# Kernel optimization log

Hardware: AMD Instinct MI355X
Metric: run time of the kernel (lower is better)

## Reference

```python
import jax, jax.numpy as jnp
import numpy as np
from jax import lax

D_MODEL = 512
D_STATE = 16
D_CONV = 4
EXPAND = 2
D_INNER = EXPAND * D_MODEL
DT_RANK = (D_MODEL + 15) // 16  # ceil(d_model/16) = 32
B = 2
L = 2048


def _silu(x):
    return x * jax.nn.sigmoid(x)


def _mamba_block(x, norm_w, norm_b, in_w, conv_w, conv_b, xproj_w, dt_w, dt_b, A_log, D_skip, out_w):
    # x: [B, L, D_MODEL]; pre-norm residual Mamba block.
    Bsz = x.shape[0]
    mu = x.mean(-1, keepdims=True)
    xc0 = x - mu
    xn = xc0 * lax.rsqrt((xc0 * xc0).mean(-1, keepdims=True) + 1e-5)
    xn = xn * norm_w + norm_b
    # in_proj (no bias): [B, L, 2*D_INNER]
    xz = jnp.einsum('bld,ed->ble', xn, in_w)
    xc, z = jnp.split(xz, 2, axis=-1)
    # depthwise causal conv over time
    xt = xc.transpose(0, 2, 1)  # [B, D_INNER, L]
    xt = lax.conv_general_dilated(xt, conv_w[:, None, :], (1,), [(D_CONV - 1, 0)],
                                  feature_group_count=D_INNER,
                                  dimension_numbers=('NCH', 'OIH', 'NCH'))
    xc = _silu((xt + conv_b[None, :, None]).transpose(0, 2, 1))  # [B, L, D_INNER]
    # x_proj -> (dt, B, C)
    dbc = jnp.einsum('bld,ed->ble', xc, xproj_w)
    dt, Bs, Cs = jnp.split(dbc, [DT_RANK, DT_RANK + D_STATE], axis=-1)
    delta = jax.nn.softplus(jnp.einsum('blr,dr->bld', dt, dt_w) + dt_b)  # [B, L, D_INNER]
    A = -jnp.exp(A_log)  # [D_INNER, D_STATE]

    def step(h, inp):
        d_t, B_t, C_t, u_t = inp  # [B,d], [B,n], [B,n], [B,d]
        h = jnp.exp(d_t[..., None] * A) * h + (d_t * u_t)[..., None] * B_t[:, None, :]
        y_t = jnp.einsum('bdn,bn->bd', h, C_t)
        return h, y_t

    xs = (delta.transpose(1, 0, 2), Bs.transpose(1, 0, 2), Cs.transpose(1, 0, 2), xc.transpose(1, 0, 2))
    h0 = jnp.zeros((Bsz, D_INNER, D_STATE), x.dtype)
    _, ys = lax.scan(step, h0, xs)
    y = ys.transpose(1, 0, 2) + xc * D_skip  # skip connection D*u
    y = y * _silu(z)
    return x + jnp.einsum('ble,de->bld', y, out_w)


def setup_inputs() -> dict:
    key = jax.random.key(0)
    ks = jax.random.split(key, 12)
    f = lambda k, shape, s=0.02: jax.random.normal(k, shape, jnp.float32) * s
    return {
        'v': jax.random.normal(ks[0], (B, L, D_MODEL), jnp.float32),
        'a': jax.random.normal(ks[1], (B, L, D_MODEL), jnp.float32),
        't': jax.random.normal(ks[2], (B, L, D_MODEL), jnp.float32),
        'norm_w': jnp.ones((3, D_MODEL), jnp.float32),
        'norm_b': jnp.zeros((3, D_MODEL), jnp.float32),
        'in_w': f(ks[3], (3, 2 * D_INNER, D_MODEL)),
        'conv_w': f(ks[4], (3, D_INNER, D_CONV), 0.1),
        'conv_b': jnp.zeros((3, D_INNER), jnp.float32),
        'xproj_w': f(ks[5], (3, DT_RANK + 2 * D_STATE, D_INNER)),
        'dt_w': f(ks[6], (3, D_INNER, DT_RANK), 0.1),
        'dt_b': jnp.full((3, D_INNER), -4.6, jnp.float32),  # softplus(-4.6) ~ 0.01
        'A_log': jnp.tile(jnp.log(jnp.arange(1, D_STATE + 1, dtype=jnp.float32)), (3, D_INNER, 1)),
        'D_skip': jnp.ones((3, D_INNER), jnp.float32),
        'out_w': f(ks[7], (3, D_MODEL, D_INNER)),
        'couple_w': f(ks[8], (3, D_MODEL, D_MODEL)),
        'coef': jnp.full((3,), 0.1, jnp.float32),  # alpha, beta, gamma
    }


def reference(v, a, t, norm_w, norm_b, in_w, conv_w, conv_b, xproj_w, dt_w, dt_b, A_log, D_skip, out_w, couple_w, coef):
    # cross-modal residual injection
    v_in = v + coef[0] * jnp.einsum('bld,ed->ble', a, couple_w[0])
    a_in = a + coef[1] * jnp.einsum('bld,ed->ble', t, couple_w[1])
    t_in = t + coef[2] * jnp.einsum('bld,ed->ble', v, couple_w[2])
    x = jnp.stack([v_in, a_in, t_in])  # [3, B, L, D]
    outs = jax.vmap(_mamba_block)(x, norm_w, norm_b, in_w, conv_w, conv_b, xproj_w,
                                  dt_w, dt_b, A_log, D_skip, out_w)
    return (outs[0], outs[1], outs[2])
```

## Files before the change

kernel.cpp:

```cpp
#include <hip/hip_runtime.h>
#include <hip/hip_bf16.h>

#define MODS 3
#define BSZ 2
#define LSEQ 2048
#define DMODEL 512
#define DINNER 1024
#define DTRANK 32
#define NSTATE 16
#define DCONV 4
#define MROWS (BSZ*LSEQ)
#define NCHUNK 64
#define CHUNK 32

#define LOG2E 1.44269504088896f
#define LN2   0.69314718055995f

typedef __attribute__((ext_vector_type(8))) short short8v;
typedef __attribute__((ext_vector_type(4))) short short4v;
typedef __attribute__((ext_vector_type(2))) short short2v;
typedef __attribute__((ext_vector_type(4))) float f32x4;

#if __has_builtin(__builtin_amdgcn_exp2f)
#define EXP2F __builtin_amdgcn_exp2f
#else
#define EXP2F exp2f
#endif
#if __has_builtin(__builtin_amdgcn_rcpf)
#define RCPF __builtin_amdgcn_rcpf
#else
#define RCPF(x) (1.0f / (x))
#endif

__device__ __forceinline__ short f2bf(float x) {
    __hip_bfloat16 h = __float2bfloat16(x);
    return __builtin_bit_cast(short, h);
}
__device__ __forceinline__ float bf2f(short s) {
    return __uint_as_float(((unsigned)(unsigned short)s) << 16);
}
__device__ __forceinline__ void gl_lds16(const short* g, short* l) {
    __builtin_amdgcn_global_load_lds(
        (const __attribute__((address_space(1))) unsigned int*)g,
        (__attribute__((address_space(3))) unsigned int*)l, 16, 0, 0);
}
__device__ __forceinline__ float sigmoid_f(float x) {
    return RCPF(1.f + EXP2F(-x * LOG2E));
}

#define MFMAQ(QR, QC)                                                              \
    _Pragma("unroll")                                                              \
    for (int rf = 0; rf < 2; ++rf)                                                 \
        _Pragma("unroll")                                                          \
        for (int cf = 0; cf < 2; ++cf)                                             \
            _Pragma("unroll")                                                      \
            for (int kh = 0; kh < 2; ++kh)                                         \
                acc[QR][QC][rf][cf] = __builtin_amdgcn_mfma_f32_16x16x32_bf16(     \
                    afr[rf][kh], bfr[cf][kh], acc[QR][QC][rf][cf], 0, 0, 0);

__global__ __launch_bounds__(1024) void gemm8p_inproj(
    const __hip_bfloat16* __restrict__ A_, const __hip_bfloat16* __restrict__ B_,
    __hip_bfloat16* __restrict__ C_)
{
    constexpr int NT = 8;
    __shared__ alignas(16) short As[2 * 16384];
    __shared__ alignas(16) short Bs[2 * 16384];
    const int z = blockIdx.z;
    const int bm0 = blockIdx.x * 256;
    const int bn0 = blockIdx.y * 256;
    const short* Ag = (const short*)A_ + (long)z * 2097152 + (long)bm0 * 512;
    const short* Bg = (const short*)B_ + (long)z * 1048576 + (long)bn0 * 512;
    short* Cg = (short*)C_ + (long)z * 8388608;
    const int tid = threadIdx.x;
    const int lane = tid & 63;
    const int w = tid >> 6;
    const int wr = w >> 2;
    const int wc = w & 3;
    const int lr = lane & 15;
    const int sidx = lane >> 4;
    const int srow_l = tid >> 3;
    const int sgoff = ((tid & 7) ^ (srow_l & 7)) * 8;

    f32x4 acc[2][2][2][2];
    #pragma unroll
    for (int a = 0; a < 2; ++a)
        #pragma unroll
        for (int b = 0; b < 2; ++b)
            #pragma unroll
            for (int c = 0; c < 2; ++c)
                #pragma unroll
                for (int d = 0; d < 2; ++d)
                    acc[a][b][c][d] = (f32x4){0.f, 0.f, 0.f, 0.f};

    short8v afr[2][2];
    short8v bfr[2][2];

    auto stageA = [&](int buf, int half, int t) {
        const int row = half * 128 + srow_l;
        gl_lds16(Ag + (long)row * 512 + t * 64 + sgoff,
                 As + buf * 16384 + half * 8192 + tid * 8);
    };
    auto stageB = [&](int buf, int half, int t) {
        const int row = half * 128 + srow_l;
        gl_lds16(Bg + (long)row * 512 + t * 64 + sgoff,
                 Bs + buf * 16384 + half * 8192 + tid * 8);
    };
    auto loadA = [&](int buf, int qr) {
        #pragma unroll
        for (int rf = 0; rf < 2; ++rf)
            #pragma unroll
            for (int kh = 0; kh < 2; ++kh) {
                const int ra = qr * 128 + wr * 32 + rf * 16 + lr;
                const int g = kh * 4 + sidx;
                afr[rf][kh] = *(const short8v*)&As[buf * 16384 + ra * 64 + ((g ^ (ra & 7)) << 3)];
            }
    };
    auto loadB = [&](int buf, int qc) {
        #pragma unroll
        for (int cf = 0; cf < 2; ++cf)
            #pragma unroll
            for (int kh = 0; kh < 2; ++kh) {
                const int rb = qc * 128 + wc * 32 + cf * 16 + lr;
                const int g = kh * 4 + sidx;
                bfr[cf][kh] = *(const short8v*)&Bs[buf * 16384 + rb * 64 + ((g ^ (rb & 7)) << 3)];
            }
    };

    stageA(0, 0, 0); stageB(0, 0, 0); stageA(0, 1, 0); stageB(0, 1, 0);

    for (int t = 0; t < NT; ++t) {
        const int p = t & 1;
        const bool stg = (t + 1) < NT;
        if (stg) { stageA(p ^ 1, 0, t + 1);
                   asm volatile("s_waitcnt vmcnt(3)" ::: "memory"); }
        else       asm volatile("s_waitcnt vmcnt(2)" ::: "memory");
        asm volatile("s_barrier" ::: "memory");
        loadA(p, 0); loadB(p, 0);
        MFMAQ(0, 0)
        asm volatile("s_barrier" ::: "memory");
        if (stg) { stageB(p ^ 1, 0, t + 1);
                   asm volatile("s_waitcnt vmcnt(3)" ::: "memory"); }
        else       asm volatile("s_waitcnt vmcnt(1)" ::: "memory");
        asm volatile("s_barrier" ::: "memory");
        loadA(p, 1);
        MFMAQ(1, 0)
        asm volatile("s_barrier" ::: "memory");
        if (stg) { stageA(p ^ 1, 1, t + 1);
                   asm volatile("s_waitcnt vmcnt(3)" ::: "memory"); }
        else       asm volatile("s_waitcnt vmcnt(0)" ::: "memory");
        asm volatile("s_barrier" ::: "memory");
        loadB(p, 1);
        MFMAQ(1, 1)
        asm volatile("s_barrier" ::: "memory");
        if (stg) stageB(p ^ 1, 1, t + 1);
        asm volatile("s_barrier" ::: "memory");
        loadA(p, 0);
        MFMAQ(0, 1)
        asm volatile("s_barrier" ::: "memory");
    }

    #pragma unroll
    for (int qr = 0; qr < 2; ++qr)
        #pragma unroll
        for (int qc = 0; qc < 2; ++qc)
            #pragma unroll
            for (int rf = 0; rf < 2; ++rf)
                #pragma unroll
                for (int r = 0; r < 4; ++r) {
                    const int row = bm0 + qr * 128 + wr * 32 + rf * 16 + (lane >> 4) * 4 + r;
                    #pragma unroll
                    for (int cf = 0; cf < 2; ++cf) {
                        const int col = bn0 + qc * 128 + wc * 32 + cf * 16 + lr;
                        Cg[(long)row * 2048 + col] = f2bf(acc[qr][qc][rf][cf][r]);
                    }
                }
}

template<int NJ, int BK>
__global__ __launch_bounds__(256) void gemm_bf16(
    const __hip_bfloat16* __restrict__ A_, const __hip_bfloat16* __restrict__ B_,
    int K, int lda, int ldb, long sA, long sB,
    float* __restrict__ Cf, __hip_bfloat16* __restrict__ Cb, int ldc, long sC,
    const float* __restrict__ res, long sRes,
    const float* __restrict__ resB, const float* __restrict__ resC,
    const __hip_bfloat16* __restrict__ resbf, long sResb,
    const float* __restrict__ coef_base, int coef_stride,
    const float* __restrict__ bias, long sBias, int act)
{
    constexpr int BN = NJ * 32;
    constexpr int ASZ = 128 * BK;
    constexpr int BSZe = BN * BK;
    __shared__ alignas(16) short As[2 * ASZ];
    __shared__ alignas(16) short Bs[2 * BSZe];
    const int z = blockIdx.z;
    const int bm0 = blockIdx.x * 128;
    const int bn0 = blockIdx.y * BN;
    const short* Ag = (const short*)A_ + z * sA + (long)bm0 * lda;
    const short* Bg = (const short*)B_ + z * sB + (long)bn0 * ldb;
    const int tid = threadIdx.x;
    const int lane = tid & 63;
    const int w = tid >> 6;
    const int wr = w >> 1, wc = w & 1;
    const int lr = lane & 15;
    const int sidx = lane >> 4;

    constexpr int SLOTS = BK / 8;
    const int srow = tid / SLOTS;
    const int sslot = tid % SLOTS;
    int swz;
    if constexpr (BK == 64) swz = srow & 7;
    else                    swz = (srow >> 1) & 3;
    const int sgcol = (sslot ^ swz) * 8;
    int fA;
    if constexpr (BK == 64) fA = lr & 7;
    else                    fA = (lr >> 1) & 3;

    constexpr int AINSTR = ASZ / 2048;
    constexpr int BINSTR = BSZe / 2048;
    constexpr int RPI = 2048 / BK;

    f32x4 acc[4][NJ];
    #pragma unroll
    for (int i = 0; i < 4; ++i)
        #pragma unroll
        for (int j = 0; j < NJ; ++j)
            acc[i][j] = (f32x4){0.f, 0.f, 0.f, 0.f};

    auto stage = [&](int buf, int k0) {
        #pragma unroll
        for (int i = 0; i < AINSTR; ++i)
            gl_lds16(Ag + (long)(i * RPI + srow) * lda + k0 + sgcol,
                     As + buf * ASZ + i * 2048 + tid * 8);
        #pragma unroll
        for (int i = 0; i < BINSTR; ++i)
            gl_lds16(Bg + (long)(i * RPI + srow) * ldb + k0 + sgcol,
                     Bs + buf * BSZe + i * 2048 + tid * 8);
    };
    auto compute = [&](int buf) {
        #pragma unroll
        for (int kh = 0; kh < BK / 32; ++kh) {
            const int sl = ((kh * 4 + sidx) ^ fA) * 8;
            short8v af[4], bfr2[NJ];
            #pragma unroll
            for (int i = 0; i < 4; ++i)
                af[i] = *(const short8v*)&As[buf * ASZ + (wr * 64 + i * 16 + lr) * BK + sl];
            #pragma unroll
            for (int j = 0; j < NJ; ++j)
                bfr2[j] = *(const short8v*)&Bs[buf * BSZe + (wc * NJ * 16 + j * 16 + lr) * BK + sl];
            #pragma unroll
            for (int i = 0; i < 4; ++i)
                #pragma unroll
                for (int j = 0; j < NJ; ++j)
                    acc[i][j] = __builtin_amdgcn_mfma_f32_16x16x32_bf16(af[i], bfr2[j], acc[i][j], 0, 0, 0);
        }
    };

    stage(0, 0);
    __syncthreads();
    int cur = 0;
    for (int k0 = BK; k0 < K; k0 += BK) {
        stage(cur ^ 1, k0);
        compute(cur);
        __syncthreads();
        cur ^= 1;
    }
    compute(cur);

    const float alpha = coef_base ? coef_base[z * coef_stride] : 1.0f;
    const float* resz = nullptr;
    if (res) {
        if (resB) resz = (z == 0) ? res : ((z == 1) ? resB : resC);
        else      resz = res + z * sRes;
    }
    const short* resbz = resbf ? (const short*)resbf + (long)z * sResb : nullptr;
    const float* biasz = bias ? bias + z * sBias : nullptr;
    float* Cfz = Cf ? Cf + (long)z * sC : nullptr;
    __hip_bfloat16* Cbz = Cb ? Cb + (long)z * sC : nullptr;
    #pragma unroll
    for (int i = 0; i < 4; ++i) {
        #pragma unroll
        for (int r = 0; r < 4; ++r) {
            const int row = bm0 + wr * 64 + i * 16 + (lane >> 4) * 4 + r;
            #pragma unroll
            for (int j = 0; j < NJ; ++j) {
                const int col = bn0 + wc * NJ * 16 + j * 16 + lr;
                float val = acc[i][j][r];
                if (biasz) val += biasz[col];
                if (act == 1)
                    val = (val > 20.f) ? val : LN2 * __log2f(1.f + EXP2F(val * LOG2E));
                val *= alpha;
                if (resz)  val += resz[(long)row * ldc + col];
                if (resbz) val += bf2f(resbz[(long)row * ldc + col]);
                if (Cfz) Cfz[(long)row * ldc + col] = val;
                else     Cbz[(long)row * ldc + col] = __float2bfloat16(val);
            }
        }
    }
}

__global__ __launch_bounds__(256) void prep_kernel(
    const float* __restrict__ a, const float* __restrict__ t, const float* __restrict__ v,
    __hip_bfloat16* __restrict__ sec_bf,
    const float* __restrict__ couple_w, __hip_bfloat16* __restrict__ cw_bf,
    const float* __restrict__ in_w, __hip_bfloat16* __restrict__ inw_bf,
    const float* __restrict__ xproj_w, __hip_bfloat16* __restrict__ xpw_bf,
    const float* __restrict__ dt_w, __hip_bfloat16* __restrict__ dtw_bf,
    const float* __restrict__ out_w, __hip_bfloat16* __restrict__ outw_bf,
    const float* __restrict__ conv_w, float* __restrict__ cwT,
    const float* __restrict__ A_log, float* __restrict__ A2T)
{
    long idx = (long)blockIdx.x * 256 + threadIdx.x;
    if (idx < 1572864) {
        const int m = (int)(idx >> 19);
        const long off = idx & 524287;
        const float* sec = (m == 0) ? a : (m == 1) ? t : v;
        float4 sv = ((const float4*)sec)[off];
        short4v s;
        s.x = f2bf(sv.x); s.y = f2bf(sv.y); s.z = f2bf(sv.z); s.w = f2bf(sv.w);
        ((short4v*)sec_bf)[idx] = s;
        return;
    }
    idx -= 1572864;
    if (idx < 1449984) {
        const float* s; __hip_bfloat16* d; long off = idx;
        if      (off < 196608)              { s = couple_w; d = cw_bf; }
        else if ((off -= 196608) < 786432)  { s = in_w;     d = inw_bf; }
        else if ((off -= 786432) < 49152)   { s = xproj_w;  d = xpw_bf; }
        else if ((off -= 49152) < 24576)    { s = dt_w;     d = dtw_bf; }
        else    { off -= 24576;               s = out_w;    d = outw_bf; }
        float4 vv = ((const float4*)s)[off];
        short4v o;
        o.x = f2bf(vv.x); o.y = f2bf(vv.y); o.z = f2bf(vv.z); o.w = f2bf(vv.w);
        ((short4v*)d)[off] = o;
        return;
    }
    idx -= 1449984;
    if (idx < 12288) {
        const int k = (int)(idx & 3);
        const int c = (int)((idx >> 2) & 1023);
        const int m = (int)(idx >> 12);
        cwT[(m * DCONV + k) * DINNER + c] = conv_w[idx];
        return;
    }
    idx -= 12288;
    if (idx < 49152) {
        const int c = (int)(idx & 1023);
        const int n = (int)((idx >> 10) & 15);
        const int m = (int)(idx >> 14);
        A2T[idx] = -EXP2F(A_log[((long)m * DINNER + c) * NSTATE + n] * LOG2E) * LOG2E;
    }
}

__global__ __launch_bounds__(256) void ln_kernel(const __hip_bfloat16* __restrict__ x,
                                                 __hip_bfloat16* __restrict__ xn,
                                                 const float* __restrict__ nw, const float* __restrict__ nb)
{
    const int row = blockIdx.x;
    const int m = row >> 12;
    const int tid = threadIdx.x;
    const short2v vv = *(const short2v*)((const short*)x + (long)row * DMODEL + tid * 2);
    const float vx = bf2f(vv.x), vy = bf2f(vv.y);
    float s = vx + vy;
    float sq = vx * vx + vy * vy;
    #pragma unroll
    for (int off = 32; off > 0; off >>= 1) {
        s  += __shfl_down(s, off);
        sq += __shfl_down(sq, off);
    }
    __shared__ float ws_s[4], ws_q[4];
    const int wid = tid >> 6, lane = tid & 63;
    if (lane == 0) { ws_s[wid] = s; ws_q[wid] = sq; }
    __syncthreads();
    if (tid == 0) {
        float ts = ws_s[0] + ws_s[1] + ws_s[2] + ws_s[3];
        float tq = ws_q[0] + ws_q[1] + ws_q[2] + ws_q[3];
        float mu = ts / DMODEL;
        float var = tq / DMODEL - mu * mu;
        ws_s[0] = mu;
        ws_q[0] = rsqrtf(var + 1e-5f);
    }
    __syncthreads();
    const float mu = ws_s[0], rstd = ws_q[0];
    const int e0 = tid * 2;
    float2 w  = *reinterpret_cast<const float2*>(nw + m * DMODEL + e0);
    float2 bb = *reinterpret_cast<const float2*>(nb + m * DMODEL + e0);
    short2v o;
    o.x = f2bf((vx - mu) * rstd * w.x + bb.x);
    o.y = f2bf((vy - mu) * rstd * w.y + bb.y);
    *reinterpret_cast<short2v*>((short*)xn + (long)row * DMODEL + e0) = o;
}

__global__ __launch_bounds__(256) void conv_silu_kernel(const __hip_bfloat16* __restrict__ xz,
    const float* __restrict__ cwT, const float* __restrict__ cb, __hip_bfloat16* __restrict__ xc)
{
    const int idx = blockIdx.x * 256 + threadIdx.x;
    const int c8 = idx & 127;
    const int lt = (idx >> 7) & 255;
    const int mb = idx >> 15;
    const int m  = mb >> 1;
    const int c0 = c8 * 8;
    const int l0 = lt * 8;

    float4 wlo[DCONV], whi[DCONV];
    #pragma unroll
    for (int k = 0; k < DCONV; ++k) {
        wlo[k] = *(const float4*)&cwT[(m * DCONV + k) * DINNER + c0];
        whi[k] = *(const float4*)&cwT[(m * DCONV + k) * DINNER + c0 + 4];
    }
    const float4 blo = *(const float4*)&cb[m * DINNER + c0];
    const float4 bhi = *(const float4*)&cb[m * DINNER + c0 + 4];

    const short* base = (const short*)xz + (long)mb * LSEQ * 2048 + c0;
    short* obase = (short*)xc + (long)mb * LSEQ * DINNER + c0;

    short8v r0 = {}, r1 = {}, r2 = {};
    if (l0 - 3 >= 0) r0 = *(const short8v*)(base + (long)(l0 - 3) * 2048);
    if (l0 - 2 >= 0) r1 = *(const short8v*)(base + (long)(l0 - 2) * 2048);
    if (l0 - 1 >= 0) r2 = *(const short8v*)(base + (long)(l0 - 1) * 2048);

    #pragma unroll
    for (int i = 0; i < 8; ++i) {
        const short8v cur = *(const short8v*)(base + (long)(l0 + i) * 2048);
        float acc[8];
        #pragma unroll
        for (int j = 0; j < 4; ++j) {
            acc[j]     = ((const float*)&blo)[j];
            acc[4 + j] = ((const float*)&bhi)[j];
        }
        #pragma unroll
        for (int j = 0; j < 8; ++j) {
            const float w0 = (j < 4) ? ((const float*)&wlo[0])[j] : ((const float*)&whi[0])[j - 4];
            const float w1 = (j < 4) ? ((const float*)&wlo[1])[j] : ((const float*)&whi[1])[j - 4];
            const float w2 = (j < 4) ? ((const float*)&wlo[2])[j] : ((const float*)&whi[2])[j - 4];
            const float w3 = (j < 4) ? ((const float*)&wlo[3])[j] : ((const float*)&whi[3])[j - 4];
            acc[j] += w0 * bf2f(r0[j]) + w1 * bf2f(r1[j]) + w2 * bf2f(r2[j]) + w3 * bf2f(cur[j]);
        }
        short8v o;
        #pragma unroll
        for (int j = 0; j < 8; ++j)
            o[j] = f2bf(acc[j] * sigmoid_f(acc[j]));
        *(short8v*)(obase + (long)(l0 + i) * DINNER) = o;
        r0 = r1; r1 = r2; r2 = cur;
    }
}

__device__ __forceinline__ bool geo_check(const float* A2) {
    bool g = true;
    #pragma unroll
    for (int n = 1; n < NSTATE; ++n)
        g = g && (__builtin_fabsf(A2[n] - (float)(n + 1) * A2[0]) <= 1e-4f * __builtin_fabsf(A2[n]));
    return g;
}

__global__ __launch_bounds__(256) void scan_pass1_kernel(
    const __hip_bfloat16* __restrict__ delta, const __hip_bfloat16* __restrict__ xc,
    const __hip_bfloat16* __restrict__ dbc, const float* __restrict__ A2T,
    float* __restrict__ Fbuf, float* __restrict__ sumd)
{
    const int bx = blockIdx.x;
    const int chunk = bx & (NCHUNK - 1);
    const int cg = (bx >> 6) & 1;
    const int mb = bx >> 7;
    const int m = mb >> 1, b = mb & 1;
    const int tid = threadIdx.x;
    const int c0 = cg * 256 + tid;
    const int c1 = c0 + 512;

    float A2a[NSTATE], A2b[NSTATE];
    #pragma unroll
    for (int n = 0; n < NSTATE; ++n) {
        A2a[n] = A2T[((long)m * NSTATE + n) * DINNER + c0];
        A2b[n] = A2T[((long)m * NSTATE + n) * DINNER + c1];
    }
    const bool geo = geo_check(A2a) && geo_check(A2b);
    float h0[NSTATE] = {}, h1[NSTATE] = {};
    float sd0 = 0.f, sd1 = 0.f;

    __shared__ float sB[CHUNK][NSTATE];
    const short* dbc_mb = (const short*)dbc + (long)m * MROWS * 64 + (long)b * LSEQ * 64;
    const int t0 = chunk * CHUNK;
    for (int i = tid; i < CHUNK * NSTATE; i += 256) {
        int tt = i >> 4, j = i & 15;
        sB[tt][j] = bf2f(dbc_mb[(long)(t0 + tt) * 64 + 32 + j]);
    }
    __syncthreads();

    const short* dp = (const short*)delta;
    const short* up = (const short*)xc;
    const long base = ((long)mb * LSEQ + t0) * DINNER + c0;
    if (geo) {
        #pragma unroll 2
        for (int tt = 0; tt < CHUNK; ++tt) {
            const long ix = base + (long)tt * DINNER;
            const float d0 = bf2f(dp[ix]),       u0 = bf2f(up[ix]);
            const float d1 = bf2f(dp[ix + 512]), u1 = bf2f(up[ix + 512]);
            const float du0 = d0 * u0, du1 = d1 * u1;
            sd0 += d0; sd1 += d1;
            const float E0 = EXP2F(d0 * A2a[0]);
            const float E1 = EXP2F(d1 * A2b[0]);
            float e0 = 1.f, e1 = 1.f;
            #pragma unroll
            for (int n = 0; n < NSTATE; ++n) {
                e0 *= E0; e1 *= E1;
                h0[n] = e0 * h0[n] + du0 * sB[tt][n];
                h1[n] = e1 * h1[n] + du1 * sB[tt][n];
            }
        }
    } else {
        #pragma unroll 2
        for (int tt = 0; tt < CHUNK; ++tt) {
            const long ix = base + (long)tt * DINNER;
            const float d0 = bf2f(dp[ix]),       u0 = bf2f(up[ix]);
            const float d1 = bf2f(dp[ix + 512]), u1 = bf2f(up[ix + 512]);
            const float du0 = d0 * u0, du1 = d1 * u1;
            sd0 += d0; sd1 += d1;
            #pragma unroll
            for (int n = 0; n < NSTATE; ++n) {
                h0[n] = EXP2F(d0 * A2a[n]) * h0[n] + du0 * sB[tt][n];
                h1[n] = EXP2F(d1 * A2b[n]) * h1[n] + du1 * sB[tt][n];
            }
        }
    }
    const long ob = ((long)mb * NCHUNK + chunk) * (NSTATE * DINNER) + c0;
    #pragma unroll
    for (int n = 0; n < NSTATE; ++n) {
        Fbuf[ob + n * DINNER] = h0[n];
        Fbuf[ob + n * DINNER + 512] = h1[n];
    }
    const long so = (((long)mb * NCHUNK + chunk) << 10) + c0;
    sumd[so] = sd0;
    sumd[so + 512] = sd1;
}

__global__ __launch_bounds__(256) void scan_pass2_kernel(float* __restrict__ Fbuf,
                                                         const float* __restrict__ sumd,
                                                         const float* __restrict__ A2T)
{
    const long idx = (long)blockIdx.x * 256 + threadIdx.x;
    const int mb = (int)(idx >> 14);
    const int cn = (int)(idx & 16383);
    const int n = cn >> 10;
    const int c = cn & 1023;
    const int m = mb >> 1;
    const float A2n = A2T[((long)m * NSTATE + n) * DINNER + c];
    float run = 0.f;
    #pragma unroll 4
    for (int k = 0; k < NCHUNK; ++k) {
        const long o = ((long)(mb * NCHUNK + k) << 14) + cn;
        const float f = Fbuf[o];
        const float p = EXP2F(sumd[(((long)mb * NCHUNK + k) << 10) + c] * A2n);
        Fbuf[o] = run;
        run = p * run + f;
    }
}

__global__ __launch_bounds__(256) void scan_pass3_kernel(
    const __hip_bfloat16* __restrict__ delta, const __hip_bfloat16* __restrict__ xc,
    const __hip_bfloat16* __restrict__ dbc, __hip_bfloat16* __restrict__ xz,
    const float* __restrict__ A2T, const float* __restrict__ D_skip,
    const float* __restrict__ Hin)
{
    const int bx = blockIdx.x;
    const int chunk = bx & (NCHUNK - 1);
    const int cg = (bx >> 6) & 1;
    const int mb = bx >> 7;
    const int m = mb >> 1, b = mb & 1;
    const int tid = threadIdx.x;
    const int c0 = cg * 256 + tid;
    const int c1 = c0 + 512;

    float A2a[NSTATE], A2b[NSTATE];
    #pragma unroll
    for (int n = 0; n < NSTATE; ++n) {
        A2a[n] = A2T[((long)m * NSTATE + n) * DINNER + c0];
        A2b[n] = A2T[((long)m * NSTATE + n) * DINNER + c1];
    }
    const bool geo = geo_check(A2a) && geo_check(A2b);
    const float Dsk0 = D_skip[m * DINNER + c0];
    const float Dsk1 = D_skip[m * DINNER + c1];

    float h0[NSTATE], h1[NSTATE];
    const long ho = ((long)mb * NCHUNK + chunk) * (NSTATE * DINNER) + c0;
    #pragma unroll
    for (int n = 0; n < NSTATE; ++n) {
        h0[n] = Hin[ho + n * DINNER];
        h1[n] = Hin[ho + n * DINNER + 512];
    }

    __shared__ float sBC[CHUNK][2 * NSTATE];
    const short* dbc_mb = (const short*)dbc + (long)m * MROWS * 64 + (long)b * LSEQ * 64;
    const int t0 = chunk * CHUNK;
    for (int i = tid; i < CHUNK * 2 * NSTATE; i += 256) {
        int tt = i >> 5, j = i & 31;
        sBC[tt][j] = bf2f(dbc_mb[(long)(t0 + tt) * 64 + 32 + j]);
    }
    __syncthreads();

    const short* dp = (const short*)delta;
    const short* up = (const short*)xc;
    short* xzp = (short*)xz;
    const long base = ((long)mb * LSEQ + t0) * DINNER + c0;
    const long xbase = ((long)mb * LSEQ + t0) * 2048 + c0;
    if (geo) {
        #pragma unroll 2
        for (int tt = 0; tt < CHUNK; ++tt) {
            const long ix = base + (long)tt * DINNER;
            const long xi = xbase + (long)tt * 2048;
            const float d0 = bf2f(dp[ix]),       u0 = bf2f(up[ix]);
            const float d1 = bf2f(dp[ix + 512]), u1 = bf2f(up[ix + 512]);
            const float zv0 = bf2f(xzp[xi + 1024]);
            const float zv1 = bf2f(xzp[xi + 1536]);
            const float du0 = d0 * u0, du1 = d1 * u1;
            const float E0 = EXP2F(d0 * A2a[0]);
            const float E1 = EXP2F(d1 * A2b[0]);
            float e0 = 1.f, e1 = 1.f;
            float y0 = 0.f, y1 = 0.f;
            #pragma unroll
            for (int n = 0; n < NSTATE; ++n) {
                e0 *= E0; e1 *= E1;
                h0[n] = e0 * h0[n] + du0 * sBC[tt][n];
                h1[n] = e1 * h1[n] + du1 * sBC[tt][n];
                y0 += h0[n] * sBC[tt][16 + n];
                y1 += h1[n] * sBC[tt][16 + n];
            }
            y0 += u0 * Dsk0;
            y1 += u1 * Dsk1;
            xzp[xi]       = f2bf(y0 * (zv0 * sigmoid_f(zv0)));
            xzp[xi + 512] = f2bf(y1 * (zv1 * sigmoid_f(zv1)));
        }
    } else {
        #pragma unroll 2
        for (int tt = 0; tt < CHUNK; ++tt) {
            const long ix = base + (long)tt * DINNER;
            const long xi = xbase + (long)tt * 2048;
            const float d0 = bf2f(dp[ix]),       u0 = bf2f(up[ix]);
            const float d1 = bf2f(dp[ix + 512]), u1 = bf2f(up[ix + 512]);
            const float zv0 = bf2f(xzp[xi + 1024]);
            const float zv1 = bf2f(xzp[xi + 1536]);
            const float du0 = d0 * u0, du1 = d1 * u1;
            float y0 = 0.f, y1 = 0.f;
            #pragma unroll
            for (int n = 0; n < NSTATE; ++n) {
                h0[n] = EXP2F(d0 * A2a[n]) * h0[n] + du0 * sBC[tt][n];
                h1[n] = EXP2F(d1 * A2b[n]) * h1[n] + du1 * sBC[tt][n];
                y0 += h0[n] * sBC[tt][16 + n];
                y1 += h1[n] * sBC[tt][16 + n];
            }
            y0 += u0 * Dsk0;
            y1 += u1 * Dsk1;
            xzp[xi]       = f2bf(y0 * (zv0 * sigmoid_f(zv0)));
            xzp[xi + 512] = f2bf(y1 * (zv1 * sigmoid_f(zv1)));
        }
    }
}

extern "C" void kernel_launch(void* const* d_in, const int* in_sizes, int n_in,
                              void* d_out, int out_size, void* d_ws, size_t ws_size,
                              hipStream_t stream)
{
    const float* v       = (const float*)d_in[0];
    const float* a       = (const float*)d_in[1];
    const float* t       = (const float*)d_in[2];
    const float* norm_w  = (const float*)d_in[3];
    const float* norm_b  = (const float*)d_in[4];
    const float* in_w    = (const float*)d_in[5];
    const float* conv_w  = (const float*)d_in[6];
    const float* conv_b  = (const float*)d_in[7];
    const float* xproj_w = (const float*)d_in[8];
    const float* dt_w    = (const float*)d_in[9];
    const float* dt_b    = (const float*)d_in[10];
    const float* A_log   = (const float*)d_in[11];
    const float* D_skip  = (const float*)d_in[12];
    const float* out_w   = (const float*)d_in[13];
    const float* couple_w= (const float*)d_in[14];
    const float* coef    = (const float*)d_in[15];
    float* out = (float*)d_out;

    typedef __hip_bfloat16 bf;
    float* ws0    = (float*)d_ws;
    bf* x_in_bf   = (bf*)ws0;
    bf* xn_bf     = (bf*)(ws0 + 6291456);
    bf* sec_bf    = xn_bf + 6291456;
    bf* xz_bf     = sec_bf + 6291456;
    bf* xc_bf     = xz_bf + 25165824;
    bf* delta_bf  = xc_bf + 12582912;
    bf* dbc_bf    = delta_bf + 12582912;
    bf* cw_bf     = dbc_bf + 786432;
    bf* inw_bf    = cw_bf + 786432;
    bf* xpw_bf    = inw_bf + 3145728;
    bf* dtw_bf    = xpw_bf + 196608;
    bf* outw_bf   = dtw_bf + 98304;
    float* cwT    = (float*)(outw_bf + 1572864);
    float* A2T    = cwT + 12288;
    float* Fbuf   = A2T + 49152;
    float* sumd   = Fbuf + 6291456;

    dim3 blk(256);

    prep_kernel<<<(1572864 + 1449984 + 12288 + 49152 + 255) / 256, blk, 0, stream>>>(
        a, t, v, sec_bf, couple_w, cw_bf, in_w, inw_bf, xproj_w, xpw_bf,
        dt_w, dtw_bf, out_w, outw_bf, conv_w, cwT, A_log, A2T);

    gemm_bf16<2, 64><<<dim3(32, 8, 3), blk, 0, stream>>>(
        sec_bf, cw_bf, 512, 512, 512, 2097152L, 262144L,
        nullptr, x_in_bf, 512, 2097152L,
        v, 0L, a, t, nullptr, 0L, coef, 1, nullptr, 0L, 0);
    ln_kernel<<<3*4096, blk, 0, stream>>>(x_in_bf, xn_bf, norm_w, norm_b);
    gemm8p_inproj<<<dim3(16, 8, 3), 1024, 0, stream>>>(xn_bf, inw_bf, xz_bf);
    conv_silu_kernel<<<768, blk, 0, stream>>>(xz_bf, cwT, conv_b, xc_bf);
    gemm_bf16<2, 64><<<dim3(32, 1, 3), blk, 0, stream>>>(
        xc_bf, xpw_bf, 1024, 1024, 1024, 4194304L, 65536L,
        nullptr, dbc_bf, 64, 262144L, nullptr, 0L, nullptr, nullptr, nullptr, 0L,
        nullptr, 0, nullptr, 0L, 0);
    gemm_bf16<4, 32><<<dim3(32, 8, 3), blk, 0, stream>>>(
        dbc_bf, dtw_bf, 32, 64, 32, 262144L, 32768L,
        nullptr, delta_bf, 1024, 4194304L, nullptr, 0L, nullptr, nullptr, nullptr, 0L,
        nullptr, 0, dt_b, 1024L, 1);
    scan_pass1_kernel<<<6*2*NCHUNK, blk, 0, stream>>>(delta_bf, xc_bf, dbc_bf, A2T, Fbuf, sumd);
    scan_pass2_kernel<<<(6*1024*16)/256, blk, 0, stream>>>(Fbuf, sumd, A2T);
    scan_pass3_kernel<<<6*2*NCHUNK, blk, 0, stream>>>(delta_bf, xc_bf, dbc_bf, xz_bf,
                                                      A2T, D_skip, Fbuf);
    gemm_bf16<2, 64><<<dim3(32, 8, 3), blk, 0, stream>>>(
        xz_bf, outw_bf, 1024, 2048, 1024, 8388608L, 524288L,
        out, nullptr, 512, 2097152L, nullptr, 0L, nullptr, nullptr, x_in_bf, 2097152L,
        nullptr, 0, nullptr, 0L, 0);
}
```

Before: 241.2 us.

## Shrink in_proj GEMM tile to 256x128 and double grid in N

The in_proj GEMM block tile drops from 256x256 to 256x128, halving the B staging buffer and accumulator registers, and the grid doubles along N (16x16x3 instead of 16x8x3). The goal is more workgroups (768 vs 384) to fill the 256 CUs better and to cut LDS/register pressure so occupancy can rise. The cost is lower per-block data reuse: each A tile is now loaded twice as often from global memory, and the four-phase pipeline is reduced to two phases with fewer barriers.

```diff
diff --git a/kernel.cpp b/kernel.cpp
--- a/kernel.cpp
+++ b/kernel.cpp
@@ -48,15 +48,15 @@
     return RCPF(1.f + EXP2F(-x * LOG2E));
 }
 
-#define MFMAQ(QR, QC)                                                              \
+#define MFMAQ(QR)                                                                  \
     _Pragma("unroll")                                                              \
     for (int rf = 0; rf < 2; ++rf)                                                 \
         _Pragma("unroll")                                                          \
         for (int cf = 0; cf < 2; ++cf)                                             \
             _Pragma("unroll")                                                      \
             for (int kh = 0; kh < 2; ++kh)                                         \
-                acc[QR][QC][rf][cf] = __builtin_amdgcn_mfma_f32_16x16x32_bf16(     \
-                    afr[rf][kh], bfr[cf][kh], acc[QR][QC][rf][cf], 0, 0, 0);
+                acc[QR][rf][cf] = __builtin_amdgcn_mfma_f32_16x16x32_bf16(         \
+                    afr[rf][kh], bfr[cf][kh], acc[QR][rf][cf], 0, 0, 0);
 
 __global__ __launch_bounds__(1024) void gemm8p_inproj(
     const __hip_bfloat16* __restrict__ A_, const __hip_bfloat16* __restrict__ B_,
@@ -64,10 +64,10 @@
 {
     constexpr int NT = 8;
     __shared__ alignas(16) short As[2 * 16384];
-    __shared__ alignas(16) short Bs[2 * 16384];
+    __shared__ alignas(16) short Bs[2 * 8192];
     const int z = blockIdx.z;
     const int bm0 = blockIdx.x * 256;
-    const int bn0 = blockIdx.y * 256;
+    const int bn0 = blockIdx.y * 128;
     const short* Ag = (const short*)A_ + (long)z * 2097152 + (long)bm0 * 512;
     const short* Bg = (const short*)B_ + (long)z * 1048576 + (long)bn0 * 512;
     short* Cg = (short*)C_ + (long)z * 8388608;
@@ -81,16 +81,14 @@
     const int srow_l = tid >> 3;
     const int sgoff = ((tid & 7) ^ (srow_l & 7)) * 8;
 
-    f32x4 acc[2][2][2][2];
+    f32x4 acc[2][2][2];
     #pragma unroll
     for (int a = 0; a < 2; ++a)
         #pragma unroll
         for (int b = 0; b < 2; ++b)
             #pragma unroll
             for (int c = 0; c < 2; ++c)
-                #pragma unroll
-                for (int d = 0; d < 2; ++d)
-                    acc[a][b][c][d] = (f32x4){0.f, 0.f, 0.f, 0.f};
+                acc[a][b][c] = (f32x4){0.f, 0.f, 0.f, 0.f};
 
     short8v afr[2][2];
     short8v bfr[2][2];
@@ -100,10 +98,10 @@
         gl_lds16(Ag + (long)row * 512 + t * 64 + sgoff,
                  As + buf * 16384 + half * 8192 + tid * 8);
     };
-    auto stageB = [&](int buf, int half, int t) {
-        const int row = half * 128 + srow_l;
+    auto stageB = [&](int buf, int t) {
+        const int row = srow_l;
         gl_lds16(Bg + (long)row * 512 + t * 64 + sgoff,
-                 Bs + buf * 16384 + half * 8192 + tid * 8);
+                 Bs + buf * 8192 + tid * 8);
     };
     auto loadA = [&](int buf, int qr) {
         #pragma unroll
@@ -115,65 +113,51 @@
                 afr[rf][kh] = *(const short8v*)&As[buf * 16384 + ra * 64 + ((g ^ (ra & 7)) << 3)];
             }
     };
-    auto loadB = [&](int buf, int qc) {
+    auto loadB = [&](int buf) {
         #pragma unroll
         for (int cf = 0; cf < 2; ++cf)
             #pragma unroll
             for (int kh = 0; kh < 2; ++kh) {
-                const int rb = qc * 128 + wc * 32 + cf * 16 + lr;
+                const int rb = wc * 32 + cf * 16 + lr;
                 const int g = kh * 4 + sidx;
-                bfr[cf][kh] = *(const short8v*)&Bs[buf * 16384 + rb * 64 + ((g ^ (rb & 7)) << 3)];
+                bfr[cf][kh] = *(const short8v*)&Bs[buf * 8192 + rb * 64 + ((g ^ (rb & 7)) << 3)];
             }
     };
 
-    stageA(0, 0, 0); stageB(0, 0, 0); stageA(0, 1, 0); stageB(0, 1, 0);
+    stageA(0, 0, 0); stageB(0, 0); stageA(0, 1, 0);
 
     for (int t = 0; t < NT; ++t) {
         const int p = t & 1;
         const bool stg = (t + 1) < NT;
-        if (stg) { stageA(p ^ 1, 0, t + 1);
-                   asm volatile("s_waitcnt vmcnt(3)" ::: "memory"); }
-        else       asm volatile("s_waitcnt vmcnt(2)" ::: "memory");
-        asm volatile("s_barrier" ::: "memory");
-        loadA(p, 0); loadB(p, 0);
-        MFMAQ(0, 0)
-        asm volatile("s_barrier" ::: "memory");
-        if (stg) { stageB(p ^ 1, 0, t + 1);
+        if (stg) { stageA(p ^ 1, 0, t + 1); stageB(p ^ 1, t + 1);
                    asm volatile("s_waitcnt vmcnt(3)" ::: "memory"); }
         else       asm volatile("s_waitcnt vmcnt(1)" ::: "memory");
         asm volatile("s_barrier" ::: "memory");
-        loadA(p, 1);
-        MFMAQ(1, 0)
+        loadA(p, 0); loadB(p);
+        MFMAQ(0)
         asm volatile("s_barrier" ::: "memory");
         if (stg) { stageA(p ^ 1, 1, t + 1);
                    asm volatile("s_waitcnt vmcnt(3)" ::: "memory"); }
         else       asm volatile("s_waitcnt vmcnt(0)" ::: "memory");
         asm volatile("s_barrier" ::: "memory");
-        loadB(p, 1);
-        MFMAQ(1, 1)
+        loadA(p, 1);
+        MFMAQ(1)
         asm volatile("s_barrier" ::: "memory");
-        if (stg) stageB(p ^ 1, 1, t + 1);
-        asm volatile("s_barrier" ::: "memory");
-        loadA(p, 0);
-        MFMAQ(0, 1)
-        asm volatile("s_barrier" ::: "memory");
     }
 
     #pragma unroll
     for (int qr = 0; qr < 2; ++qr)
         #pragma unroll
-        for (int qc = 0; qc < 2; ++qc)
-            #pragma unroll
-            for (int rf = 0; rf < 2; ++rf)
+        for (int rf = 0; rf < 2; ++rf)
+            #pragma unroll
+            for (int r = 0; r < 4; ++r) {
+                const int row = bm0 + qr * 128 + wr * 32 + rf * 16 + (lane >> 4) * 4 + r;
                 #pragma unroll
-                for (int r = 0; r < 4; ++r) {
-                    const int row = bm0 + qr * 128 + wr * 32 + rf * 16 + (lane >> 4) * 4 + r;
-                    #pragma unroll
-                    for (int cf = 0; cf < 2; ++cf) {
-                        const int col = bn0 + qc * 128 + wc * 32 + cf * 16 + lr;
-                        Cg[(long)row * 2048 + col] = f2bf(acc[qr][qc][rf][cf][r]);
-                    }
+                for (int cf = 0; cf < 2; ++cf) {
+                    const int col = bn0 + wc * 32 + cf * 16 + lr;
+                    Cg[(long)row * 2048 + col] = f2bf(acc[qr][rf][cf][r]);
                 }
+            }
 }
 
 template<int NJ, int BK>
@@ -706,7 +690,7 @@
         nullptr, x_in_bf, 512, 2097152L,
         v, 0L, a, t, nullptr, 0L, coef, 1, nullptr, 0L, 0);
     ln_kernel<<<3*4096, blk, 0, stream>>>(x_in_bf, xn_bf, norm_w, norm_b);
-    gemm8p_inproj<<<dim3(16, 8, 3), 1024, 0, stream>>>(xn_bf, inw_bf, xz_bf);
+    gemm8p_inproj<<<dim3(16, 16, 3), 1024, 0, stream>>>(xn_bf, inw_bf, xz_bf);
     conv_silu_kernel<<<768, blk, 0, stream>>>(xz_bf, cwT, conv_b, xc_bf);
     gemm_bf16<2, 64><<<dim3(32, 1, 3), blk, 0, stream>>>(
         xc_bf, xpw_bf, 1024, 1024, 1024, 4194304L, 65536L,
```

Result: no change. 238.2 us (-1.2%).
